# Kernel tuning notes

Measured on AMD Instinct MI355X. Metric: run time of the kernel, lower is better.

Reference implementation:

```python
import jax, jax.numpy as jnp
import numpy as np

N = 16384      # nodes (radar cells x batched graphs)
H = 128        # n_hidden
N_ENV = 7
N_IN = N_ENV + 2 + 1  # env + coords + density = 10
T_CTX = 24
HORIZON = 40
T = T_CTX + HORIZON


def setup_inputs() -> dict:
    key = jax.random.key(0)
    ks = jax.random.split(key, 40)

    def w(k, shape, fan_in):
        return jax.random.normal(k, shape, jnp.float32) * np.float32(1.0 / np.sqrt(fan_in))

    inp = {}
    inp["x"] = jax.random.normal(ks[0], (N, T), jnp.float32)
    inp["coords"] = jax.random.normal(ks[1], (N, 2), jnp.float32)
    inp["env"] = jax.random.normal(ks[2], (N, N_ENV, T), jnp.float32)
    # --- encoder params ---
    inp["enc_W_in"] = w(ks[3], (H, N_IN), N_IN)           # Linear(n_in->H), no bias
    inp["enc_Wih0"] = w(ks[4], (4 * H, H), H)
    inp["enc_Whh0"] = w(ks[5], (4 * H, H), H)
    inp["enc_bih0"] = jnp.zeros((4 * H,), jnp.float32)
    inp["enc_bhh0"] = jnp.zeros((4 * H,), jnp.float32)
    inp["enc_Wih1"] = w(ks[6], (4 * H, H), H)
    inp["enc_Whh1"] = w(ks[7], (4 * H, H), H)
    inp["enc_bih1"] = jnp.zeros((4 * H,), jnp.float32)
    inp["enc_bhh1"] = jnp.zeros((4 * H,), jnp.float32)
    # --- NodeLSTM params ---
    inp["node_W_in"] = w(ks[8], (H, N_IN), N_IN)          # Linear(n_in->H), no bias
    inp["in_Wih"] = w(ks[9], (4 * H, 2 * H), 2 * H)       # lstm_in takes [inputs, enc_state]
    inp["in_Whh"] = w(ks[10], (4 * H, H), H)
    inp["in_bih"] = jnp.zeros((4 * H,), jnp.float32)
    inp["in_bhh"] = jnp.zeros((4 * H,), jnp.float32)
    inp["l1_Wih"] = w(ks[11], (4 * H, H), H)
    inp["l1_Whh"] = w(ks[12], (4 * H, H), H)
    inp["l1_bih"] = jnp.zeros((4 * H,), jnp.float32)
    inp["l1_bhh"] = jnp.zeros((4 * H,), jnp.float32)
    # hidden2in / hidden2out heads: Linear(H,H) -> ReLU -> Linear(H,1)
    inp["h2in_W1"] = w(ks[13], (H, H), H)
    inp["h2in_b1"] = jnp.zeros((H,), jnp.float32)
    inp["h2in_W2"] = w(ks[14], (1, H), H)
    inp["h2in_b2"] = jnp.zeros((1,), jnp.float32)
    inp["h2out_W1"] = w(ks[15], (H, H), H)
    inp["h2out_b1"] = jnp.zeros((H,), jnp.float32)
    inp["h2out_W2"] = w(ks[16], (1, H), H)
    inp["h2out_b2"] = jnp.zeros((1,), jnp.float32)
    return inp


def _lstm_cell(xin, h, c, Wih, Whh, bih, bhh):
    # torch.nn.LSTMCell semantics; gate order i, f, g, o
    gates = xin @ Wih.T + h @ Whh.T + (bih + bhh)
    i, f, g, o = jnp.split(gates, 4, axis=1)
    c_new = jax.nn.sigmoid(f) * c + jax.nn.sigmoid(i) * jnp.tanh(g)
    h_new = jax.nn.sigmoid(o) * jnp.tanh(c_new)
    return h_new, c_new


def reference(x, coords, env,
              enc_W_in, enc_Wih0, enc_Whh0, enc_bih0, enc_bhh0,
              enc_Wih1, enc_Whh1, enc_bih1, enc_bhh1,
              node_W_in, in_Wih, in_Whh, in_bih, in_bhh,
              l1_Wih, l1_Whh, l1_bih, l1_bhh,
              h2in_W1, h2in_b1, h2in_W2, h2in_b2,
              h2out_W1, h2out_b1, h2out_W2, h2out_b2):
    n = x.shape[0]
    z = jnp.zeros((n, H), x.dtype)

    # ---------- encoder: scan over T_CTX context steps ----------
    def enc_step(carry, xs):
        h0, c0, h1, c1 = carry
        xt, et = xs  # [N], [N, N_ENV]
        inp = jnp.concatenate([xt[:, None], coords, et], axis=1) @ enc_W_in.T
        h0, c0 = _lstm_cell(inp, h0, c0, enc_Wih0, enc_Whh0, enc_bih0, enc_bhh0)
        h1, c1 = _lstm_cell(h0, h1, c1, enc_Wih1, enc_Whh1, enc_bih1, enc_bhh1)
        return (h0, c0, h1, c1), None

    enc_xs = (x[:, :T_CTX].T, jnp.moveaxis(env[:, :, :T_CTX], 2, 0))
    (h0, c0, h1, c1), _ = jax.lax.scan(enc_step, (z, z, z, z), enc_xs)
    enc_state = h1  # h[-1] captured at setup_states, fixed over the horizon

    def head(hid, W1, b1, W2, b2):
        return jax.nn.sigmoid(jax.nn.relu(hid @ W1.T + b1) @ W2.T + b2)

    # ---------- decoder: scan over HORIZON forecast steps ----------
    def dec_step(carry, et):
        xc, h0, c0, h1, c1 = carry
        inp = jnp.concatenate([xc, coords, et], axis=1) @ node_W_in.T
        inp = jnp.concatenate([inp, enc_state], axis=1)  # [N, 2H]
        h0, c0 = _lstm_cell(inp, h0, c0, in_Wih, in_Whh, in_bih, in_bhh)
        h1, c1 = _lstm_cell(h0, h1, c1, l1_Wih, l1_Whh, l1_bih, l1_bhh)
        x_in = head(h1, h2in_W1, h2in_b1, h2in_W2, h2in_b2)
        x_out = head(h1, h2out_W1, h2out_b1, h2out_W2, h2out_b2)
        xn = xc + x_in - x_out * xc  # source/sink update, [N, 1]
        return (xn, h0, c0, h1, c1), xn

    x0 = x[:, T_CTX - 1][:, None]
    dec_xs = jnp.moveaxis(env[:, :, T_CTX:T_CTX + HORIZON], 2, 0)
    _, ys = jax.lax.scan(dec_step, (x0, h0, c0, h1, c1), dec_xs)  # [HORIZON, N, 1]
    return jnp.transpose(ys[..., 0], (1, 0))  # [N, HORIZON]
```

## Files before the change

### kernel.cpp

```cpp
#include <hip/hip_runtime.h>
#include <hip/hip_bf16.h>
#include <cstdint>
#include <cstddef>

typedef __bf16 bf16_t;
typedef bf16_t bf16x8 __attribute__((ext_vector_type(8)));
typedef bf16_t bf16x4 __attribute__((ext_vector_type(4)));
typedef float  f32x4  __attribute__((ext_vector_type(4)));

#define TT    64
#define T_CTX 24
#define HOR   40
#define SA    264
#define NTH   512

#define MFMA __builtin_amdgcn_mfma_f32_16x16x32_bf16

#define O_PKE   16
#define O_PKD   (O_PKE + 262144)
#define O_PKX   (O_PKD + 294912)
#define O_BIAS  (O_PKX + 131072)
#define O_HEADP (O_BIAS + 2048)
#define O_WINE  (O_HEADP + 512)
#define O_WINN  (O_WINE + 1536)
#define O_B2    (O_WINN + 1536)

struct Ptrs { const void* q[29]; };

__device__ __forceinline__ float sigm(float x) {
  return __builtin_amdgcn_rcpf(1.f + __expf(-x));
}
__device__ __forceinline__ float tanh_(float x) {
  return 1.f - 2.f * __builtin_amdgcn_rcpf(1.f + __expf(2.f * x));
}
__device__ __forceinline__ unsigned pk2(float a, float b) {
  unsigned ua = __float_as_uint(a), ub = __float_as_uint(b);
  ua = (ua + 0x7fffu + ((ua >> 16) & 1u)) >> 16;
  ub = (ub + 0x7fffu + ((ub >> 16) & 1u)) >> 16;
  return ua | (ub << 16);
}
__device__ __forceinline__ float uplo(unsigned p){ return __uint_as_float(p << 16); }
__device__ __forceinline__ float uphi(unsigned p){ return __uint_as_float(p & 0xffff0000u); }

__global__ void detect_kernel(const unsigned short* __restrict__ wsrc, int* __restrict__ flag)
{
  int tid = threadIdx.x;
  int wild = 0;
  for (int i = tid; i < 256; i += 64) {
    unsigned short b = wsrc[i];
    float v  = __uint_as_float(((unsigned)b) << 16);
    float av = fabsf(v);
    unsigned e = (b >> 7) & 0xff;
    if (av > 1000.f || e == 0xff || (((b & 0x7fff) != 0) && av < 1e-9f)) wild++;
  }
  for (int off = 32; off; off >>= 1) wild += __shfl_down(wild, off, 64);
  if (tid == 0) flag[0] = (wild > 16) ? 1 : 0;
}

__global__ void prep_kernel(Ptrs P, bf16_t* __restrict__ wb, const int* __restrict__ flag)
{
  const bool f32 = (flag[0] != 0);
  const int gtid = blockIdx.x * blockDim.x + threadIdx.x;
  const int gsz  = gridDim.x * blockDim.x;
  auto rd = [&](const void* src, int i) -> float {
    return f32 ? ((const float*)src)[i] : (float)((const bf16_t*)src)[i];
  };

  for (int i = gtid; i < 262144; i += gsz) {
    int w = i >> 15, r = i & 32767, f = r >> 9, e = r & 511;
    int ln = e >> 3, j = e & 7;
    int seg = f >> 5, fk = f & 31, kt = fk >> 2, g = fk & 3;
    int row = g * 128 + w * 16 + (ln & 15);
    int col = kt * 32 + ((ln >> 4) << 3) + j;
    float v;
    if (seg == 0) v = (col < 128) ? rd(P.q[4], row * 128 + col) : rd(P.q[5], row * 128 + col - 128);
    else          v = (col < 128) ? rd(P.q[8], row * 128 + col) : rd(P.q[9], row * 128 + col - 128);
    wb[O_PKE + i] = (bf16_t)v;
  }
  for (int i = gtid; i < 294912; i += gsz) {
    int w = i / 36864, r = i - w * 36864, f = r >> 9, e = r & 511;
    int ln = e >> 3, j = e & 7;
    int colk = ((ln >> 4) << 3) + j;
    float v;
    if (f < 64) {
      int seg = f >> 5, fk = f & 31, kt = fk >> 2, g = fk & 3;
      int row = g * 128 + w * 16 + (ln & 15);
      int col = kt * 32 + colk;
      if (seg == 0) v = (col < 128) ? rd(P.q[13], row * 256 + col) : rd(P.q[14], row * 128 + col - 128);
      else          v = (col < 128) ? rd(P.q[17], row * 128 + col) : rd(P.q[18], row * 128 + col - 128);
    } else {
      int f2 = f - 64, h = f2 >> 2, kt = f2 & 3;
      int row = w * 16 + (ln & 15);
      int col = kt * 32 + colk;
      v = rd(h ? P.q[25] : P.q[21], row * 128 + col);
    }
    wb[O_PKD + i] = (bf16_t)v;
  }
  for (int i = gtid; i < 131072; i += gsz) {
    int w = i >> 14, r = i & 16383, f = r >> 9, e = r & 511;
    int ln = e >> 3, j = e & 7;
    int kt = f >> 2, g = f & 3;
    int row = g * 128 + w * 16 + (ln & 15);
    int col = kt * 32 + ((ln >> 4) << 3) + j;
    wb[O_PKX + i] = (bf16_t)rd(P.q[13], row * 256 + 128 + col);
  }
  for (int i = gtid; i < 512; i += gsz) {
    wb[O_BIAS + i]        = (bf16_t)(rd(P.q[6],  i) + rd(P.q[7],  i));
    wb[O_BIAS + 512 + i]  = (bf16_t)(rd(P.q[10], i) + rd(P.q[11], i));
    wb[O_BIAS + 1024 + i] = (bf16_t)(rd(P.q[15], i) + rd(P.q[16], i));
    wb[O_BIAS + 1536 + i] = (bf16_t)(rd(P.q[19], i) + rd(P.q[20], i));
  }
  for (int i = gtid; i < 128; i += gsz) {
    wb[O_HEADP + i]       = (bf16_t)rd(P.q[22], i);
    wb[O_HEADP + 128 + i] = (bf16_t)rd(P.q[23], i);
    wb[O_HEADP + 256 + i] = (bf16_t)rd(P.q[26], i);
    wb[O_HEADP + 384 + i] = (bf16_t)rd(P.q[27], i);
  }
  for (int i = gtid; i < 1536; i += gsz) {
    int cc = i / 12, j = i % 12;
    wb[O_WINE + i] = (j < 10) ? (bf16_t)rd(P.q[3],  cc * 10 + j) : (bf16_t)0.f;
    wb[O_WINN + i] = (j < 10) ? (bf16_t)rd(P.q[12], cc * 10 + j) : (bf16_t)0.f;
  }
  if (gtid == 0) {
    wb[O_B2]     = (bf16_t)rd(P.q[24], 0);
    wb[O_B2 + 1] = (bf16_t)rd(P.q[28], 0);
  }
}

struct PreB { bf16x8 b[2][4]; };

__device__ __forceinline__ PreB preB(const bf16_t* __restrict__ pl) {
  PreB r;
#pragma unroll
  for (int p = 0; p < 2; ++p)
#pragma unroll
    for (int g = 0; g < 4; ++g)
      r.b[p][g] = *(const bf16x8*)(pl + (p * 4 + g) * 512);
  return r;
}

template<int NKT>
__device__ __forceinline__ void gemm_pk(f32x4 (&acc)[4][4], const bf16_t* __restrict__ As,
                                        const bf16_t* __restrict__ pl, const PreB& pre,
                                        int l, int q)
{
  bf16x8 bw[3][4];
#pragma unroll
  for (int g = 0; g < 4; ++g) { bw[0][g] = pre.b[0][g]; bw[1][g] = pre.b[1][g]; }
#pragma unroll
  for (int kt = 0; kt < NKT; ++kt) {
    bf16x8 a[4];
#pragma unroll
    for (int mt = 0; mt < 4; ++mt)
      a[mt] = *(const bf16x8*)(As + (mt * 16 + l) * SA + kt * 32 + q * 8);
    if (kt + 2 < NKT) {
#pragma unroll
      for (int g = 0; g < 4; ++g)
        bw[(kt + 2) % 3][g] = *(const bf16x8*)(pl + ((kt + 2) * 4 + g) * 512);
    }
#pragma unroll
    for (int g = 0; g < 4; ++g) {
      bf16x8 b = bw[kt % 3][g];
      acc[g][0] = MFMA(a[0], b, acc[g][0], 0, 0, 0);
      acc[g][1] = MFMA(a[1], b, acc[g][1], 0, 0, 0);
      acc[g][2] = MFMA(a[2], b, acc[g][2], 0, 0, 0);
      acc[g][3] = MFMA(a[3], b, acc[g][3], 0, 0, 0);
    }
  }
}

template<bool DUAL>
__device__ __forceinline__ void cell_up(f32x4 (&acc)[4][4], float (&c)[16],
                                        bf16_t* __restrict__ shb, bf16_t* __restrict__ sha,
                                        const bf16_t* __restrict__ bias,
                                        int wid, int l, int q)
{
  const int jc = wid * 16 + l;
  const float bi  = (float)bias[jc];
  const float bf_ = (float)bias[128 + jc];
  const float bg  = (float)bias[256 + jc];
  const float bo  = (float)bias[384 + jc];
#pragma unroll
  for (int mt = 0; mt < 4; ++mt) {
#pragma unroll
    for (int r = 0; r < 4; ++r) {
      float gi = acc[0][mt][r] + bi;
      float gf = acc[1][mt][r] + bf_;
      float gg = acc[2][mt][r] + bg;
      float go = acc[3][mt][r] + bo;
      float cn = sigm(gf) * c[mt * 4 + r] + sigm(gi) * tanh_(gg);
      float hh = sigm(go) * tanh_(cn);
      c[mt * 4 + r] = cn;
      const int row = mt * 16 + q * 4 + r;
      shb[row * SA + jc] = (bf16_t)hh;
      if (DUAL) sha[row * SA + jc] = (bf16_t)hh;
    }
  }
}

__device__ __forceinline__ void proj16(const float* v, const bf16_t* __restrict__ wbase,
                                       bf16_t* __restrict__ sx, int nd, int sub)
{
  bf16x8 o0, o1;
#pragma unroll
  for (int cc = 0; cc < 16; ++cc) {
    const bf16_t* wr = wbase + (sub * 16 + cc) * 12;
    bf16x4 w0 = *(const bf16x4*)(wr);
    bf16x4 w1 = *(const bf16x4*)(wr + 4);
    bf16x4 w2 = *(const bf16x4*)(wr + 8);
    float a = v[0] * (float)w0[0] + v[1] * (float)w0[1] + v[2] * (float)w0[2] + v[3] * (float)w0[3]
            + v[4] * (float)w1[0] + v[5] * (float)w1[1] + v[6] * (float)w1[2] + v[7] * (float)w1[3]
            + v[8] * (float)w2[0] + v[9] * (float)w2[1];
    if (cc < 8) o0[cc] = (bf16_t)a; else o1[cc - 8] = (bf16_t)a;
  }
  *(bf16x8*)(sx + nd * SA + sub * 16)     = o0;
  *(bf16x8*)(sx + nd * SA + sub * 16 + 8) = o1;
}

template<typename T>
__global__ __launch_bounds__(NTH, 1) void lstm_persist(
    const T* __restrict__ x, const T* __restrict__ coords, const T* __restrict__ env,
    const bf16_t* __restrict__ w, const int* __restrict__ flag, T* __restrict__ out)
{
  const bool want_f32 = (sizeof(T) == 4);
  if ((flag[0] != 0) != want_f32) return;

  __shared__ __align__(16) bf16_t bufA[64 * SA];
  __shared__ __align__(16) bf16_t bufB[64 * SA];
  __shared__ __align__(16) bf16_t s_win[2 * 128 * 12];
  __shared__ __align__(16) bf16_t s_bias[4 * 512];
  __shared__ float s_red[128];
  __shared__ float s_xc[64];

  const int tid  = threadIdx.x;
  const int wid  = tid >> 6;
  const int lane = tid & 63;
  const int l    = tid & 15;
  const int q    = (tid & 63) >> 4;
  const int node0 = blockIdx.x * 64;
  const int nd  = tid >> 3;
  const int sub = tid & 7;

  const bf16_t* plE0 = w + O_PKE + wid * 32768 + lane * 8;
  const bf16_t* plE1 = plE0 + 16384;
  const bf16_t* plD0 = w + O_PKD + wid * 36864 + lane * 8;
  const bf16_t* plD1 = plD0 + 16384;
  const bf16_t* plH  = plD0 + 32768;
  const bf16_t* plX  = w + O_PKX + wid * 16384 + lane * 8;

  for (int i = tid; i < 2048; i += NTH) s_bias[i] = w[O_BIAS + i];
  for (int i = tid; i < 3072; i += NTH) s_win[i]  = w[O_WINE + i];
  for (int i = tid; i < 64 * SA; i += NTH) { bufA[i] = (bf16_t)0.f; bufB[i] = (bf16_t)0.f; }

  const float cx = (float)coords[(size_t)(node0 + nd) * 2 + 0];
  const float cy = (float)coords[(size_t)(node0 + nd) * 2 + 1];

  float c0[16], c1[16];
#pragma unroll
  for (int i = 0; i < 16; ++i) { c0[i] = 0.f; c1[i] = 0.f; }

  PreB pA = preB(plE0);
  __syncthreads();

#pragma unroll 1
  for (int t = 0; t < T_CTX; ++t) {
    float v[10];
    v[0] = (float)x[(size_t)(node0 + nd) * TT + t];
    v[1] = cx; v[2] = cy;
#pragma unroll
    for (int e = 0; e < 7; ++e)
      v[3 + e] = (float)env[((size_t)(node0 + nd) * 7 + e) * TT + t];
    proj16(v, s_win, bufA, nd, sub);
    __syncthreads();

    f32x4 acc[4][4];
#pragma unroll
    for (int g = 0; g < 4; ++g)
#pragma unroll
      for (int mt = 0; mt < 4; ++mt) acc[g][mt] = f32x4{0.f, 0.f, 0.f, 0.f};
    gemm_pk<8>(acc, bufA, plE0, pA, l, q);
    PreB pC = preB(plE1);
    __syncthreads();
    cell_up<true>(acc, c0, bufB, bufA + 128, s_bias, wid, l, q);
    __syncthreads();

#pragma unroll
    for (int g = 0; g < 4; ++g)
#pragma unroll
      for (int mt = 0; mt < 4; ++mt) acc[g][mt] = f32x4{0.f, 0.f, 0.f, 0.f};
    gemm_pk<8>(acc, bufB, plE1, pC, l, q);
    pA = preB((t < T_CTX - 1) ? plE0 : plX);
    __syncthreads();
    cell_up<false>(acc, c1, bufB + 128, nullptr, s_bias + 512, wid, l, q);
  }
  __syncthreads();

  uint2 geh[4][4];
  {
    f32x4 acc[4][4];
#pragma unroll
    for (int g = 0; g < 4; ++g)
#pragma unroll
      for (int mt = 0; mt < 4; ++mt) acc[g][mt] = f32x4{0.f, 0.f, 0.f, 0.f};
    gemm_pk<4>(acc, bufB + 128, plX, pA, l, q);
#pragma unroll
    for (int g = 0; g < 4; ++g)
#pragma unroll
      for (int mt = 0; mt < 4; ++mt)
        geh[g][mt] = uint2{pk2(acc[g][mt][0], acc[g][mt][1]),
                           pk2(acc[g][mt][2], acc[g][mt][3])};
  }
  if (tid < 64) s_xc[tid] = (float)x[(size_t)(node0 + tid) * TT + (T_CTX - 1)];
  const float b2i = (float)w[O_B2];
  const float b2o = (float)w[O_B2 + 1];
  const float b1i = (float)w[O_HEADP + wid * 16 + l];
  const float w2i = (float)w[O_HEADP + 128 + wid * 16 + l];
  const float b1o = (float)w[O_HEADP + 256 + wid * 16 + l];
  const float w2o = (float)w[O_HEADP + 384 + wid * 16 + l];
  pA = preB(plD0);
  __syncthreads();

#pragma unroll 1
  for (int s = 0; s < HOR; ++s) {
    const int t = T_CTX + s;
    float v[10];
    v[0] = s_xc[nd];
    v[1] = cx; v[2] = cy;
#pragma unroll
    for (int e = 0; e < 7; ++e)
      v[3 + e] = (float)env[((size_t)(node0 + nd) * 7 + e) * TT + t];
    proj16(v, s_win + 1536, bufA, nd, sub);
    __syncthreads();

    f32x4 acc[4][4];
#pragma unroll
    for (int g = 0; g < 4; ++g)
#pragma unroll
      for (int mt = 0; mt < 4; ++mt)
        acc[g][mt] = f32x4{uplo(geh[g][mt].x), uphi(geh[g][mt].x),
                           uplo(geh[g][mt].y), uphi(geh[g][mt].y)};
    gemm_pk<8>(acc, bufA, plD0, pA, l, q);
    PreB pC = preB(plD1);
    __syncthreads();
    cell_up<true>(acc, c0, bufB, bufA + 128, s_bias + 1024, wid, l, q);
    __syncthreads();

#pragma unroll
    for (int g = 0; g < 4; ++g)
#pragma unroll
      for (int mt = 0; mt < 4; ++mt) acc[g][mt] = f32x4{0.f, 0.f, 0.f, 0.f};
    gemm_pk<8>(acc, bufB, plD1, pC, l, q);
    bf16x8 hb[8];
#pragma unroll
    for (int f = 0; f < 8; ++f) hb[f] = *(const bf16x8*)(plH + f * 512);
    __syncthreads();
    cell_up<false>(acc, c1, bufB + 128, nullptr, s_bias + 1536, wid, l, q);
    if (tid < 128) s_red[tid] = 0.f;
    pA = preB(plD0);
    __syncthreads();

    f32x4 hacc[2][4];
#pragma unroll
    for (int hd = 0; hd < 2; ++hd)
#pragma unroll
      for (int mt = 0; mt < 4; ++mt) hacc[hd][mt] = f32x4{0.f, 0.f, 0.f, 0.f};
#pragma unroll
    for (int kt = 0; kt < 4; ++kt) {
      bf16x8 a[4];
#pragma unroll
      for (int mt = 0; mt < 4; ++mt)
        a[mt] = *(const bf16x8*)(bufB + 128 + (mt * 16 + l) * SA + kt * 32 + q * 8);
#pragma unroll
      for (int mt = 0; mt < 4; ++mt) {
        hacc[0][mt] = MFMA(a[mt], hb[kt],     hacc[0][mt], 0, 0, 0);
        hacc[1][mt] = MFMA(a[mt], hb[4 + kt], hacc[1][mt], 0, 0, 0);
      }
    }
#pragma unroll
    for (int hd = 0; hd < 2; ++hd) {
      const float b1v = hd ? b1o : b1i;
      const float w2v = hd ? w2o : w2i;
#pragma unroll
      for (int mt = 0; mt < 4; ++mt)
#pragma unroll
        for (int r = 0; r < 4; ++r) {
          float val = fmaxf(hacc[hd][mt][r] + b1v, 0.f) * w2v;
          val += __shfl_xor(val, 1, 64);
          val += __shfl_xor(val, 2, 64);
          val += __shfl_xor(val, 4, 64);
          val += __shfl_xor(val, 8, 64);
          if (l == 0) atomicAdd(&s_red[hd * 64 + mt * 16 + q * 4 + r], val);
        }
    }
    __syncthreads();
    if (tid < 64) {
      float xc = s_xc[tid];
      float si = sigm(s_red[tid] + b2i);
      float so = sigm(s_red[64 + tid] + b2o);
      float xn = xc + si - so * xc;
      s_xc[tid] = xn;
      out[(size_t)(node0 + tid) * HOR + s] = (T)xn;
    }
    __syncthreads();
  }
}

extern "C" void kernel_launch(void* const* d_in, const int* in_sizes, int n_in,
                              void* d_out, int out_size, void* d_ws, size_t ws_size,
                              hipStream_t stream) {
  (void)in_sizes; (void)n_in; (void)out_size; (void)ws_size;
  Ptrs P;
  for (int i = 0; i < 29; ++i) P.q[i] = d_in[i];
  int*    flag = (int*)d_ws;
  bf16_t* w    = (bf16_t*)d_ws;

  detect_kernel<<<1, 64, 0, stream>>>((const unsigned short*)d_in[4], flag);
  prep_kernel<<<256, 256, 0, stream>>>(P, w, flag);
  lstm_persist<float><<<256, NTH, 0, stream>>>(
      (const float*)d_in[0], (const float*)d_in[1], (const float*)d_in[2],
      w, flag, (float*)d_out);
  lstm_persist<bf16_t><<<256, NTH, 0, stream>>>(
      (const bf16_t*)d_in[0], (const bf16_t*)d_in[1], (const bf16_t*)d_in[2],
      w, flag, (bf16_t*)d_out);
}
```

Measured before the change: 2.162 ms.

## Fold input projection into first LSTM weights and restructure per-gate GEMM passes

The 10->128 input Linear is algebraically folded into the layer-0 input weights during prep, so each step feeds the raw 10 features (padded to one 32-wide K tile) straight into the gate GEMM. This removes the per-step proj16 pass and shrinks K for layer 0 from 256 to 160. The GEMM is restructured into per-gate passes with B fragments software-prefetched a gate ahead. The encoder-state gate contribution moves from registers into shared memory, and next-step x/env loads are issued early. Folding in fp32 then casting the product to bf16 changes rounding slightly and raises LDS use.

```diff
diff --git a/kernel.cpp b/kernel.cpp
--- a/kernel.cpp
+++ b/kernel.cpp
@@ -5,25 +5,23 @@
 
 typedef __bf16 bf16_t;
 typedef bf16_t bf16x8 __attribute__((ext_vector_type(8)));
-typedef bf16_t bf16x4 __attribute__((ext_vector_type(4)));
 typedef float  f32x4  __attribute__((ext_vector_type(4)));
 
 #define TT    64
 #define T_CTX 24
 #define HOR   40
-#define SA    264
+#define SL0   168
+#define SL1   264
 #define NTH   512
 
 #define MFMA __builtin_amdgcn_mfma_f32_16x16x32_bf16
 
 #define O_PKE   16
-#define O_PKD   (O_PKE + 262144)
-#define O_PKX   (O_PKD + 294912)
-#define O_BIAS  (O_PKX + 131072)
+#define O_PKD   (O_PKE + 212992)
+#define O_PKX   (O_PKD + 245760)
+#define O_BIAS  (O_PKX + 65536)
 #define O_HEADP (O_BIAS + 2048)
-#define O_WINE  (O_HEADP + 512)
-#define O_WINN  (O_WINE + 1536)
-#define O_B2    (O_WINN + 1536)
+#define O_B2    (O_HEADP + 512)
 
 struct Ptrs { const void* q[29]; };
 
@@ -65,44 +63,64 @@
   auto rd = [&](const void* src, int i) -> float {
     return f32 ? ((const float*)src)[i] : (float)((const bf16_t*)src)[i];
   };
-
-  for (int i = gtid; i < 262144; i += gsz) {
-    int w = i >> 15, r = i & 32767, f = r >> 9, e = r & 511;
-    int ln = e >> 3, j = e & 7;
-    int seg = f >> 5, fk = f & 31, kt = fk >> 2, g = fk & 3;
-    int row = g * 128 + w * 16 + (ln & 15);
-    int col = kt * 32 + ((ln >> 4) << 3) + j;
-    float v;
-    if (seg == 0) v = (col < 128) ? rd(P.q[4], row * 128 + col) : rd(P.q[5], row * 128 + col - 128);
-    else          v = (col < 128) ? rd(P.q[8], row * 128 + col) : rd(P.q[9], row * 128 + col - 128);
-    wb[O_PKE + i] = (bf16_t)v;
-  }
-  for (int i = gtid; i < 294912; i += gsz) {
-    int w = i / 36864, r = i - w * 36864, f = r >> 9, e = r & 511;
+  auto foldE = [&](int row, int c) -> float {
+    float a = 0.f;
+    for (int k = 0; k < 128; ++k) a += rd(P.q[4], row * 128 + k) * rd(P.q[3], k * 10 + c);
+    return a;
+  };
+  auto foldD = [&](int row, int c) -> float {
+    float a = 0.f;
+    for (int k = 0; k < 128; ++k) a += rd(P.q[13], row * 256 + k) * rd(P.q[12], k * 10 + c);
+    return a;
+  };
+
+  for (int i = gtid; i < 212992; i += gsz) {
+    int w = i / 26624, r = i % 26624, f = r >> 9, e = r & 511;
     int ln = e >> 3, j = e & 7;
     int colk = ((ln >> 4) << 3) + j;
     float v;
-    if (f < 64) {
-      int seg = f >> 5, fk = f & 31, kt = fk >> 2, g = fk & 3;
+    if (f < 20) {
+      int g = f / 5, kt = f % 5;
       int row = g * 128 + w * 16 + (ln & 15);
-      int col = kt * 32 + colk;
-      if (seg == 0) v = (col < 128) ? rd(P.q[13], row * 256 + col) : rd(P.q[14], row * 128 + col - 128);
-      else          v = (col < 128) ? rd(P.q[17], row * 128 + col) : rd(P.q[18], row * 128 + col - 128);
+      if (kt == 0) v = (colk < 10) ? foldE(row, colk) : 0.f;
+      else         v = rd(P.q[5], row * 128 + (kt - 1) * 32 + colk);
     } else {
-      int f2 = f - 64, h = f2 >> 2, kt = f2 & 3;
+      int f2 = f - 20, g = f2 >> 3, kt = f2 & 7;
+      int row = g * 128 + w * 16 + (ln & 15);
+      v = (kt < 4) ? rd(P.q[8], row * 128 + kt * 32 + colk)
+                   : rd(P.q[9], row * 128 + (kt - 4) * 32 + colk);
+    }
+    wb[O_PKE + i] = (bf16_t)v;
+  }
+  for (int i = gtid; i < 245760; i += gsz) {
+    int w = i / 30720, r = i % 30720, f = r >> 9, e = r & 511;
+    int ln = e >> 3, j = e & 7;
+    int colk = ((ln >> 4) << 3) + j;
+    float v;
+    if (f < 20) {
+      int g = f / 5, kt = f % 5;
+      int row = g * 128 + w * 16 + (ln & 15);
+      if (kt == 0) v = (colk < 10) ? foldD(row, colk) : 0.f;
+      else         v = rd(P.q[14], row * 128 + (kt - 1) * 32 + colk);
+    } else if (f < 52) {
+      int f2 = f - 20, g = f2 >> 3, kt = f2 & 7;
+      int row = g * 128 + w * 16 + (ln & 15);
+      v = (kt < 4) ? rd(P.q[17], row * 128 + kt * 32 + colk)
+                   : rd(P.q[18], row * 128 + (kt - 4) * 32 + colk);
+    } else {
+      int f2 = f - 52, h = f2 >> 2, kt = f2 & 3;
       int row = w * 16 + (ln & 15);
-      int col = kt * 32 + colk;
-      v = rd(h ? P.q[25] : P.q[21], row * 128 + col);
+      v = rd(h ? P.q[25] : P.q[21], row * 128 + kt * 32 + colk);
     }
     wb[O_PKD + i] = (bf16_t)v;
   }
-  for (int i = gtid; i < 131072; i += gsz) {
-    int w = i >> 14, r = i & 16383, f = r >> 9, e = r & 511;
+  for (int i = gtid; i < 65536; i += gsz) {
+    int w = i >> 13, r = i & 8191, f = r >> 9, e = r & 511;
     int ln = e >> 3, j = e & 7;
-    int kt = f >> 2, g = f & 3;
+    int colk = ((ln >> 4) << 3) + j;
+    int g = f >> 2, kt = f & 3;
     int row = g * 128 + w * 16 + (ln & 15);
-    int col = kt * 32 + ((ln >> 4) << 3) + j;
-    wb[O_PKX + i] = (bf16_t)rd(P.q[13], row * 256 + 128 + col);
+    wb[O_PKX + i] = (bf16_t)rd(P.q[13], row * 256 + 128 + kt * 32 + colk);
   }
   for (int i = gtid; i < 512; i += gsz) {
     wb[O_BIAS + i]        = (bf16_t)(rd(P.q[6],  i) + rd(P.q[7],  i));
@@ -116,62 +134,34 @@
     wb[O_HEADP + 256 + i] = (bf16_t)rd(P.q[26], i);
     wb[O_HEADP + 384 + i] = (bf16_t)rd(P.q[27], i);
   }
-  for (int i = gtid; i < 1536; i += gsz) {
-    int cc = i / 12, j = i % 12;
-    wb[O_WINE + i] = (j < 10) ? (bf16_t)rd(P.q[3],  cc * 10 + j) : (bf16_t)0.f;
-    wb[O_WINN + i] = (j < 10) ? (bf16_t)rd(P.q[12], cc * 10 + j) : (bf16_t)0.f;
-  }
   if (gtid == 0) {
     wb[O_B2]     = (bf16_t)rd(P.q[24], 0);
     wb[O_B2 + 1] = (bf16_t)rd(P.q[28], 0);
   }
 }
 
-struct PreB { bf16x8 b[2][4]; };
-
-__device__ __forceinline__ PreB preB(const bf16_t* __restrict__ pl) {
-  PreB r;
-#pragma unroll
-  for (int p = 0; p < 2; ++p)
-#pragma unroll
-    for (int g = 0; g < 4; ++g)
-      r.b[p][g] = *(const bf16x8*)(pl + (p * 4 + g) * 512);
-  return r;
-}
-
-template<int NKT>
-__device__ __forceinline__ void gemm_pk(f32x4 (&acc)[4][4], const bf16_t* __restrict__ As,
-                                        const bf16_t* __restrict__ pl, const PreB& pre,
-                                        int l, int q)
-{
-  bf16x8 bw[3][4];
-#pragma unroll
-  for (int g = 0; g < 4; ++g) { bw[0][g] = pre.b[0][g]; bw[1][g] = pre.b[1][g]; }
+template<int NF>
+__device__ __forceinline__ void ldF(bf16x8 (&d)[NF], const bf16_t* __restrict__ pl, int f0) {
+#pragma unroll
+  for (int i = 0; i < NF; ++i) d[i] = *(const bf16x8*)(pl + (f0 + i) * 512);
+}
+
+template<int NKT, int SS>
+__device__ __forceinline__ void gpass(f32x4 (&ac)[4], const bf16_t* __restrict__ As,
+                                      const bf16x8 (&bf)[NKT], int l, int q) {
 #pragma unroll
   for (int kt = 0; kt < NKT; ++kt) {
-    bf16x8 a[4];
-#pragma unroll
-    for (int mt = 0; mt < 4; ++mt)
-      a[mt] = *(const bf16x8*)(As + (mt * 16 + l) * SA + kt * 32 + q * 8);
-    if (kt + 2 < NKT) {
-#pragma unroll
-      for (int g = 0; g < 4; ++g)
-        bw[(kt + 2) % 3][g] = *(const bf16x8*)(pl + ((kt + 2) * 4 + g) * 512);
-    }
-#pragma unroll
-    for (int g = 0; g < 4; ++g) {
-      bf16x8 b = bw[kt % 3][g];
-      acc[g][0] = MFMA(a[0], b, acc[g][0], 0, 0, 0);
-      acc[g][1] = MFMA(a[1], b, acc[g][1], 0, 0, 0);
-      acc[g][2] = MFMA(a[2], b, acc[g][2], 0, 0, 0);
-      acc[g][3] = MFMA(a[3], b, acc[g][3], 0, 0, 0);
+#pragma unroll
+    for (int mt = 0; mt < 4; ++mt) {
+      bf16x8 a = *(const bf16x8*)(As + (mt * 16 + l) * SS + kt * 32 + q * 8);
+      ac[mt] = MFMA(a, bf[kt], ac[mt], 0, 0, 0);
     }
   }
 }
 
 template<bool DUAL>
 __device__ __forceinline__ void cell_up(f32x4 (&acc)[4][4], float (&c)[16],
-                                        bf16_t* __restrict__ shb, bf16_t* __restrict__ sha,
+                                        bf16_t* __restrict__ s1, bf16_t* __restrict__ s0,
                                         const bf16_t* __restrict__ bias,
                                         int wid, int l, int q)
 {
@@ -192,30 +182,14 @@
       float hh = sigm(go) * tanh_(cn);
       c[mt * 4 + r] = cn;
       const int row = mt * 16 + q * 4 + r;
-      shb[row * SA + jc] = (bf16_t)hh;
-      if (DUAL) sha[row * SA + jc] = (bf16_t)hh;
-    }
-  }
-}
-
-__device__ __forceinline__ void proj16(const float* v, const bf16_t* __restrict__ wbase,
-                                       bf16_t* __restrict__ sx, int nd, int sub)
-{
-  bf16x8 o0, o1;
-#pragma unroll
-  for (int cc = 0; cc < 16; ++cc) {
-    const bf16_t* wr = wbase + (sub * 16 + cc) * 12;
-    bf16x4 w0 = *(const bf16x4*)(wr);
-    bf16x4 w1 = *(const bf16x4*)(wr + 4);
-    bf16x4 w2 = *(const bf16x4*)(wr + 8);
-    float a = v[0] * (float)w0[0] + v[1] * (float)w0[1] + v[2] * (float)w0[2] + v[3] * (float)w0[3]
-            + v[4] * (float)w1[0] + v[5] * (float)w1[1] + v[6] * (float)w1[2] + v[7] * (float)w1[3]
-            + v[8] * (float)w2[0] + v[9] * (float)w2[1];
-    if (cc < 8) o0[cc] = (bf16_t)a; else o1[cc - 8] = (bf16_t)a;
-  }
-  *(bf16x8*)(sx + nd * SA + sub * 16)     = o0;
-  *(bf16x8*)(sx + nd * SA + sub * 16 + 8) = o1;
-}
+      s1[row * SL1 + jc] = (bf16_t)hh;
+      if (DUAL) s0[row * SL0 + jc] = (bf16_t)hh;
+    }
+  }
+}
+
+#define ZACC(A) _Pragma("unroll") for (int _g = 0; _g < 4; ++_g) \
+                _Pragma("unroll") for (int _m = 0; _m < 4; ++_m) A[_g][_m] = f32x4{0.f,0.f,0.f,0.f};
 
 template<typename T>
 __global__ __launch_bounds__(NTH, 1) void lstm_persist(
@@ -225,10 +199,10 @@
   const bool want_f32 = (sizeof(T) == 4);
   if ((flag[0] != 0) != want_f32) return;
 
-  __shared__ __align__(16) bf16_t bufA[64 * SA];
-  __shared__ __align__(16) bf16_t bufB[64 * SA];
-  __shared__ __align__(16) bf16_t s_win[2 * 128 * 12];
-  __shared__ __align__(16) bf16_t s_bias[4 * 512];
+  __shared__ __align__(16) bf16_t s_l0[64 * SL0];
+  __shared__ __align__(16) bf16_t s_l1[64 * SL1];
+  __shared__ __align__(16) bf16_t s_bias[2048];
+  __shared__ __align__(16) unsigned s_ge[NTH * 36];
   __shared__ float s_red[128];
   __shared__ float s_xc[64];
 
@@ -238,144 +212,167 @@
   const int l    = tid & 15;
   const int q    = (tid & 63) >> 4;
   const int node0 = blockIdx.x * 64;
-  const int nd  = tid >> 3;
-  const int sub = tid & 7;
-
-  const bf16_t* plE0 = w + O_PKE + wid * 32768 + lane * 8;
-  const bf16_t* plE1 = plE0 + 16384;
-  const bf16_t* plD0 = w + O_PKD + wid * 36864 + lane * 8;
-  const bf16_t* plD1 = plD0 + 16384;
-  const bf16_t* plH  = plD0 + 32768;
-  const bf16_t* plX  = w + O_PKX + wid * 16384 + lane * 8;
+
+  const bf16_t* plE = w + O_PKE + wid * 26624 + lane * 8;
+  const bf16_t* plD = w + O_PKD + wid * 30720 + lane * 8;
+  const bf16_t* plX = w + O_PKX + wid * 8192  + lane * 8;
 
   for (int i = tid; i < 2048; i += NTH) s_bias[i] = w[O_BIAS + i];
-  for (int i = tid; i < 3072; i += NTH) s_win[i]  = w[O_WINE + i];
-  for (int i = tid; i < 64 * SA; i += NTH) { bufA[i] = (bf16_t)0.f; bufB[i] = (bf16_t)0.f; }
-
-  const float cx = (float)coords[(size_t)(node0 + nd) * 2 + 0];
-  const float cy = (float)coords[(size_t)(node0 + nd) * 2 + 1];
+  for (int i = tid; i < 64 * SL0; i += NTH) s_l0[i] = (bf16_t)0.f;
+  for (int i = tid; i < 64 * SL1; i += NTH) s_l1[i] = (bf16_t)0.f;
+
+  const T* xb = x   + (size_t)(node0 + tid) * TT;
+  const T* eb = env + (size_t)(node0 + tid) * 7 * TT;
+  float cx = 0.f, cy = 0.f, pfx = 0.f;
+  float pfe[7];
+#pragma unroll
+  for (int e = 0; e < 7; ++e) pfe[e] = 0.f;
+  if (tid < 64) {
+    cx  = (float)coords[(size_t)(node0 + tid) * 2 + 0];
+    cy  = (float)coords[(size_t)(node0 + tid) * 2 + 1];
+    pfx = (float)xb[0];
+#pragma unroll
+    for (int e = 0; e < 7; ++e) pfe[e] = (float)eb[e * TT];
+  }
 
   float c0[16], c1[16];
 #pragma unroll
   for (int i = 0; i < 16; ++i) { c0[i] = 0.f; c1[i] = 0.f; }
 
-  PreB pA = preB(plE0);
+  bf16x8 bg0[5];  ldF<5>(bg0, plE, 0);
+  bf16x8 bX0[4];
+  __syncthreads();
+  if (tid < 64) {
+    s_l0[tid * SL0 + 0] = (bf16_t)pfx;
+    s_l0[tid * SL0 + 1] = (bf16_t)cx;
+    s_l0[tid * SL0 + 2] = (bf16_t)cy;
+#pragma unroll
+    for (int e = 0; e < 7; ++e) s_l0[tid * SL0 + 3 + e] = (bf16_t)pfe[e];
+  }
   __syncthreads();
 
 #pragma unroll 1
   for (int t = 0; t < T_CTX; ++t) {
-    float v[10];
-    v[0] = (float)x[(size_t)(node0 + nd) * TT + t];
-    v[1] = cx; v[2] = cy;
-#pragma unroll
-    for (int e = 0; e < 7; ++e)
-      v[3 + e] = (float)env[((size_t)(node0 + nd) * 7 + e) * TT + t];
-    proj16(v, s_win, bufA, nd, sub);
-    __syncthreads();
-
-    f32x4 acc[4][4];
+    f32x4 acc[4][4]; ZACC(acc)
+    bf16x8 bg1[5]; ldF<5>(bg1, plE, 5);
+    gpass<5, SL0>(acc[0], s_l0, bg0, l, q);
+    bf16x8 bg2[5]; ldF<5>(bg2, plE, 10);
+    gpass<5, SL0>(acc[1], s_l0, bg1, l, q);
+    bf16x8 bg3[5]; ldF<5>(bg3, plE, 15);
+    gpass<5, SL0>(acc[2], s_l0, bg2, l, q);
+    bf16x8 h1g0[8]; ldF<8>(h1g0, plE, 20);
+    gpass<5, SL0>(acc[3], s_l0, bg3, l, q);
+    __syncthreads();
+    cell_up<true>(acc, c0, s_l1, s_l0 + 32, s_bias, wid, l, q);
+    bf16x8 h1g1[8]; ldF<8>(h1g1, plE, 28);
+    __syncthreads();
+    ZACC(acc)
+    bf16x8 h1g2[8]; ldF<8>(h1g2, plE, 36);
+    gpass<8, SL1>(acc[0], s_l1, h1g0, l, q);
+    bf16x8 h1g3[8]; ldF<8>(h1g3, plE, 44);
+    gpass<8, SL1>(acc[1], s_l1, h1g1, l, q);
+    if (tid < 64) {
+      if (t + 1 < T_CTX) pfx = (float)xb[t + 1];
+#pragma unroll
+      for (int e = 0; e < 7; ++e) pfe[e] = (float)eb[e * TT + t + 1];
+    }
+    gpass<8, SL1>(acc[2], s_l1, h1g2, l, q);
+    if (t < T_CTX - 1) ldF<5>(bg0, plE, 0);
+    else               ldF<4>(bX0, plX, 0);
+    gpass<8, SL1>(acc[3], s_l1, h1g3, l, q);
+    __syncthreads();
+    cell_up<false>(acc, c1, s_l1 + 128, nullptr, s_bias + 512, wid, l, q);
+    if (tid < 64 && t < T_CTX - 1) {
+      s_l0[tid * SL0 + 0] = (bf16_t)pfx;
+      s_l0[tid * SL0 + 1] = (bf16_t)cx;
+      s_l0[tid * SL0 + 2] = (bf16_t)cy;
+#pragma unroll
+      for (int e = 0; e < 7; ++e) s_l0[tid * SL0 + 3 + e] = (bf16_t)pfe[e];
+    }
+    __syncthreads();
+  }
+
+  {
+    f32x4 acc[4][4]; ZACC(acc)
+    bf16x8 bX1[4]; ldF<4>(bX1, plX, 4);
+    gpass<4, SL1>(acc[0], s_l1 + 128, bX0, l, q);
+    bf16x8 bX2[4]; ldF<4>(bX2, plX, 8);
+    gpass<4, SL1>(acc[1], s_l1 + 128, bX1, l, q);
+    bf16x8 bX3[4]; ldF<4>(bX3, plX, 12);
+    gpass<4, SL1>(acc[2], s_l1 + 128, bX2, l, q);
+    gpass<4, SL1>(acc[3], s_l1 + 128, bX3, l, q);
 #pragma unroll
     for (int g = 0; g < 4; ++g)
 #pragma unroll
-      for (int mt = 0; mt < 4; ++mt) acc[g][mt] = f32x4{0.f, 0.f, 0.f, 0.f};
-    gemm_pk<8>(acc, bufA, plE0, pA, l, q);
-    PreB pC = preB(plE1);
-    __syncthreads();
-    cell_up<true>(acc, c0, bufB, bufA + 128, s_bias, wid, l, q);
-    __syncthreads();
-
-#pragma unroll
-    for (int g = 0; g < 4; ++g)
-#pragma unroll
-      for (int mt = 0; mt < 4; ++mt) acc[g][mt] = f32x4{0.f, 0.f, 0.f, 0.f};
-    gemm_pk<8>(acc, bufB, plE1, pC, l, q);
-    pA = preB((t < T_CTX - 1) ? plE0 : plX);
-    __syncthreads();
-    cell_up<false>(acc, c1, bufB + 128, nullptr, s_bias + 512, wid, l, q);
-  }
-  __syncthreads();
-
-  uint2 geh[4][4];
-  {
-    f32x4 acc[4][4];
-#pragma unroll
-    for (int g = 0; g < 4; ++g)
-#pragma unroll
-      for (int mt = 0; mt < 4; ++mt) acc[g][mt] = f32x4{0.f, 0.f, 0.f, 0.f};
-    gemm_pk<4>(acc, bufB + 128, plX, pA, l, q);
-#pragma unroll
-    for (int g = 0; g < 4; ++g)
-#pragma unroll
-      for (int mt = 0; mt < 4; ++mt)
-        geh[g][mt] = uint2{pk2(acc[g][mt][0], acc[g][mt][1]),
-                           pk2(acc[g][mt][2], acc[g][mt][3])};
-  }
-  if (tid < 64) s_xc[tid] = (float)x[(size_t)(node0 + tid) * TT + (T_CTX - 1)];
+      for (int mt = 0; mt < 4; ++mt) {
+        s_ge[tid * 36 + (g * 4 + mt) * 2 + 0] = pk2(acc[g][mt][0], acc[g][mt][1]);
+        s_ge[tid * 36 + (g * 4 + mt) * 2 + 1] = pk2(acc[g][mt][2], acc[g][mt][3]);
+      }
+  }
+  if (tid < 64) {
+    s_xc[tid] = pfx;
+    s_l0[tid * SL0 + 0] = (bf16_t)pfx;
+#pragma unroll
+    for (int e = 0; e < 7; ++e) s_l0[tid * SL0 + 3 + e] = (bf16_t)pfe[e];
+  }
   const float b2i = (float)w[O_B2];
   const float b2o = (float)w[O_B2 + 1];
   const float b1i = (float)w[O_HEADP + wid * 16 + l];
   const float w2i = (float)w[O_HEADP + 128 + wid * 16 + l];
   const float b1o = (float)w[O_HEADP + 256 + wid * 16 + l];
   const float w2o = (float)w[O_HEADP + 384 + wid * 16 + l];
-  pA = preB(plD0);
+  ldF<5>(bg0, plD, 0);
   __syncthreads();
 
 #pragma unroll 1
   for (int s = 0; s < HOR; ++s) {
     const int t = T_CTX + s;
-    float v[10];
-    v[0] = s_xc[nd];
-    v[1] = cx; v[2] = cy;
-#pragma unroll
-    for (int e = 0; e < 7; ++e)
-      v[3 + e] = (float)env[((size_t)(node0 + nd) * 7 + e) * TT + t];
-    proj16(v, s_win + 1536, bufA, nd, sub);
-    __syncthreads();
-
     f32x4 acc[4][4];
 #pragma unroll
     for (int g = 0; g < 4; ++g)
 #pragma unroll
-      for (int mt = 0; mt < 4; ++mt)
-        acc[g][mt] = f32x4{uplo(geh[g][mt].x), uphi(geh[g][mt].x),
-                           uplo(geh[g][mt].y), uphi(geh[g][mt].y)};
-    gemm_pk<8>(acc, bufA, plD0, pA, l, q);
-    PreB pC = preB(plD1);
-    __syncthreads();
-    cell_up<true>(acc, c0, bufB, bufA + 128, s_bias + 1024, wid, l, q);
-    __syncthreads();
-
-#pragma unroll
-    for (int g = 0; g < 4; ++g)
-#pragma unroll
-      for (int mt = 0; mt < 4; ++mt) acc[g][mt] = f32x4{0.f, 0.f, 0.f, 0.f};
-    gemm_pk<8>(acc, bufB, plD1, pC, l, q);
-    bf16x8 hb[8];
-#pragma unroll
-    for (int f = 0; f < 8; ++f) hb[f] = *(const bf16x8*)(plH + f * 512);
-    __syncthreads();
-    cell_up<false>(acc, c1, bufB + 128, nullptr, s_bias + 1536, wid, l, q);
+      for (int mt = 0; mt < 4; ++mt) {
+        unsigned u0 = s_ge[tid * 36 + (g * 4 + mt) * 2 + 0];
+        unsigned u1 = s_ge[tid * 36 + (g * 4 + mt) * 2 + 1];
+        acc[g][mt] = f32x4{uplo(u0), uphi(u0), uplo(u1), uphi(u1)};
+      }
+    bf16x8 bg1[5]; ldF<5>(bg1, plD, 5);
+    gpass<5, SL0>(acc[0], s_l0, bg0, l, q);
+    bf16x8 bg2[5]; ldF<5>(bg2, plD, 10);
+    gpass<5, SL0>(acc[1], s_l0, bg1, l, q);
+    bf16x8 bg3[5]; ldF<5>(bg3, plD, 15);
+    gpass<5, SL0>(acc[2], s_l0, bg2, l, q);
+    bf16x8 h1g0[8]; ldF<8>(h1g0, plD, 20);
+    gpass<5, SL0>(acc[3], s_l0, bg3, l, q);
+    __syncthreads();
+    cell_up<true>(acc, c0, s_l1, s_l0 + 32, s_bias + 1024, wid, l, q);
+    bf16x8 h1g1[8]; ldF<8>(h1g1, plD, 28);
+    __syncthreads();
+    ZACC(acc)
+    bf16x8 h1g2[8]; ldF<8>(h1g2, plD, 36);
+    gpass<8, SL1>(acc[0], s_l1, h1g0, l, q);
+    bf16x8 h1g3[8]; ldF<8>(h1g3, plD, 44);
+    gpass<8, SL1>(acc[1], s_l1, h1g1, l, q);
+    bf16x8 hbi[4], hbo[4];
+    ldF<4>(hbi, plD, 52);
+    ldF<4>(hbo, plD, 56);
+    gpass<8, SL1>(acc[2], s_l1, h1g2, l, q);
+    if (tid < 64) {
+      const int tn = (t + 1 < TT) ? t + 1 : t;
+#pragma unroll
+      for (int e = 0; e < 7; ++e) pfe[e] = (float)eb[e * TT + tn];
+    }
+    gpass<8, SL1>(acc[3], s_l1, h1g3, l, q);
+    __syncthreads();
+    cell_up<false>(acc, c1, s_l1 + 128, nullptr, s_bias + 1536, wid, l, q);
     if (tid < 128) s_red[tid] = 0.f;
-    pA = preB(plD0);
-    __syncthreads();
-
-    f32x4 hacc[2][4];
-#pragma unroll
-    for (int hd = 0; hd < 2; ++hd)
-#pragma unroll
-      for (int mt = 0; mt < 4; ++mt) hacc[hd][mt] = f32x4{0.f, 0.f, 0.f, 0.f};
-#pragma unroll
-    for (int kt = 0; kt < 4; ++kt) {
-      bf16x8 a[4];
-#pragma unroll
-      for (int mt = 0; mt < 4; ++mt)
-        a[mt] = *(const bf16x8*)(bufB + 128 + (mt * 16 + l) * SA + kt * 32 + q * 8);
-#pragma unroll
-      for (int mt = 0; mt < 4; ++mt) {
-        hacc[0][mt] = MFMA(a[mt], hb[kt],     hacc[0][mt], 0, 0, 0);
-        hacc[1][mt] = MFMA(a[mt], hb[4 + kt], hacc[1][mt], 0, 0, 0);
-      }
-    }
+    __syncthreads();
+    f32x4 hi[4], ho[4];
+#pragma unroll
+    for (int m = 0; m < 4; ++m) { hi[m] = f32x4{0.f,0.f,0.f,0.f}; ho[m] = f32x4{0.f,0.f,0.f,0.f}; }
+    gpass<4, SL1>(hi, s_l1 + 128, hbi, l, q);
+    gpass<4, SL1>(ho, s_l1 + 128, hbo, l, q);
+    ldF<5>(bg0, plD, 0);
 #pragma unroll
     for (int hd = 0; hd < 2; ++hd) {
       const float b1v = hd ? b1o : b1i;
@@ -384,7 +381,7 @@
       for (int mt = 0; mt < 4; ++mt)
 #pragma unroll
         for (int r = 0; r < 4; ++r) {
-          float val = fmaxf(hacc[hd][mt][r] + b1v, 0.f) * w2v;
+          float val = fmaxf((hd ? ho[mt][r] : hi[mt][r]) + b1v, 0.f) * w2v;
           val += __shfl_xor(val, 1, 64);
           val += __shfl_xor(val, 2, 64);
           val += __shfl_xor(val, 4, 64);
@@ -400,6 +397,11 @@
       float xn = xc + si - so * xc;
       s_xc[tid] = xn;
       out[(size_t)(node0 + tid) * HOR + s] = (T)xn;
+      s_l0[tid * SL0 + 0] = (bf16_t)xn;
+      s_l0[tid * SL0 + 1] = (bf16_t)cx;
+      s_l0[tid * SL0 + 2] = (bf16_t)cy;
+#pragma unroll
+      for (int e = 0; e < 7; ++e) s_l0[tid * SL0 + 3 + e] = (bf16_t)pfe[e];
     }
     __syncthreads();
   }
@@ -419,7 +421,7 @@
   lstm_persist<float><<<256, NTH, 0, stream>>>(
       (const float*)d_in[0], (const float*)d_in[1], (const float*)d_in[2],
       w, flag, (float*)d_out);
-  lstm_persist<bf16_t><<<256, NTH, 0, stream>>>(
-      (const bf16_t*)d_in[0], (const bf16_t*)d_in[1], (const bf16_t*)d_in[2],
-      w, flag, (bf16_t*)d_out);
-}
+  lstm_persist<__bf16><<<256, NTH, 0, stream>>>(
+      (const __bf16*)d_in[0], (const __bf16*)d_in[1], (const __bf16*)d_in[2],
+      w, flag, (__bf16*)d_out);
+}
```

New measurement: 2.883 ms. 33.4% more time.
